# Performance work log

Hardware: AMD Instinct MI355X
Metric: run time of the kernel (lower is better)

The kernel has to match this reference:

```python
import jax, jax.numpy as jnp
import numpy as np

KV_H, Q_H, ATT_H = 256, 256, 128
B, S, SQ = 2, 1024, 512

def setup_inputs() -> dict:
    key = jax.random.key(0)
    ks = jax.random.split(key, 8)
    sc = lambda d: 1.0 / np.sqrt(d)
    return {
        "attention_kv": jax.random.normal(ks[0], (B, S, KV_H), dtype=jnp.float32),
        "attention_query": jax.random.normal(ks[1], (B, SQ, Q_H), dtype=jnp.float32),
        "W_kv": jax.random.uniform(ks[2], (KV_H, ATT_H), jnp.float32, -sc(KV_H), sc(KV_H)),
        "b_kv": jax.random.uniform(ks[3], (ATT_H,), jnp.float32, -sc(KV_H), sc(KV_H)),
        "W_q": jax.random.uniform(ks[4], (Q_H, ATT_H), jnp.float32, -sc(Q_H), sc(Q_H)),
        "b_q": jax.random.uniform(ks[5], (ATT_H,), jnp.float32, -sc(Q_H), sc(Q_H)),
        "w_v": jax.random.uniform(ks[6], (ATT_H,), jnp.float32, -sc(ATT_H), sc(ATT_H)),
        "b_v": jax.random.uniform(ks[7], (), jnp.float32, -sc(ATT_H), sc(ATT_H)),
    }

def reference(attention_kv, attention_query, W_kv, b_kv, W_q, b_q, w_v, b_v):
    # proj_kv: (B, S, A); proj_q: (B, Sq, A)
    proj_kv = jnp.einsum('bsh,ha->bsa', attention_kv, W_kv) + b_kv
    proj_q = jnp.einsum('bqh,ha->bqa', attention_query, W_q) + b_q
    # broadcast add + tanh -> (B, Sq, S, A)
    hidden = jnp.tanh(proj_kv[:, None, :, :] + proj_q[:, :, None, :])
    # scalar score per (b, q, s)
    attention_score = jnp.einsum('bqsa,a->bqs', hidden, w_v) + b_v
    attention_weight = jax.nn.softmax(attention_score, axis=-1)
    # weighted sum over kv sequence -> (B, Sq, KV_H)
    attention_output = jnp.einsum('bqs,bsh->bqh', attention_weight, attention_kv)
    return attention_output, attention_weight
```

## Files before the change

### kernel.cpp

```cpp
#include <hip/hip_runtime.h>
#include <hip/hip_bf16.h>

#define NB   2
#define SKV  1024
#define NSQ  512
#define HIN  256
#define HA   128

#define KSC   2.8853900817779268f
#define LOG2E 1.4426950408889634f

__global__ __launch_bounds__(128) void proj_kernel(
    const float* __restrict__ kv,
    const float* __restrict__ qy,
    const float* __restrict__ Wkv,
    const float* __restrict__ bkv,
    const float* __restrict__ Wq,
    const float* __restrict__ bq,
    float* __restrict__ pk,
    float* __restrict__ pq)
{
    __shared__ __align__(16) float rowf[8][HIN];
    const int t  = threadIdx.x;
    const int r0 = blockIdx.x * 8;
    const bool is_q = (r0 >= NB * SKV);
    const float* __restrict__ src = is_q ? (qy + (size_t)(r0 - NB * SKV) * HIN)
                                         : (kv + (size_t)r0 * HIN);
    const float* __restrict__ W  = is_q ? Wq : Wkv;
    const float* __restrict__ bs = is_q ? bq : bkv;
    float* __restrict__ dst = is_q ? (pq + (size_t)(r0 - NB * SKV) * HA)
                                   : (pk + (size_t)r0 * HA);

    const float4* __restrict__ s4 = (const float4*)src;
    float4* r4 = (float4*)&rowf[0][0];
    #pragma unroll
    for (int i = 0; i < 4; ++i) r4[t + i * 128] = s4[t + i * 128];
    __syncthreads();

    float a[8];
    #pragma unroll
    for (int i = 0; i < 8; ++i) a[i] = 0.f;
    #pragma unroll 4
    for (int h = 0; h < HIN; ++h) {
        float w = W[h * HA + t];
        #pragma unroll
        for (int i = 0; i < 8; ++i) a[i] = fmaf(rowf[i][h], w, a[i]);
    }
    const float bb = bs[t];
    #pragma unroll
    for (int i = 0; i < 8; ++i) dst[i * HA + t] = (a[i] + bb) * KSC;
}

__global__ __launch_bounds__(512) void attn_kernel(
    const float* __restrict__ pk,
    const float* __restrict__ pq,
    const float* __restrict__ wv,
    const float* __restrict__ bv,
    const float* __restrict__ kv,
    float* __restrict__ out)
{
    __shared__ __align__(16) float eq_s[4][HA];
    __shared__ __align__(16) float wv_s[HA];
    __shared__ __align__(16) float wt_s[SKV][4];
    __shared__ float red[2][4][8];
    __shared__ float w0red[8];
    __shared__ __align__(16) float part[8][4][HIN];

    const int tid  = threadIdx.x;
    const int lane = tid & 63, wid = tid >> 6;
    const int bq0  = blockIdx.x * 4;
    const int b    = bq0 >> 9;

    {
        const int row = tid >> 7, a = tid & 127;
        eq_s[row][a] = __builtin_amdgcn_exp2f(pq[(size_t)(bq0 + row) * HA + a]);
    }
    float w0p = (tid < HA) ? wv[tid] : 0.f;
    if (tid < HA) wv_s[tid] = w0p;
    #pragma unroll
    for (int o = 32; o > 0; o >>= 1) w0p += __shfl_down(w0p, o);
    if (lane == 0) w0red[wid] = w0p;
    const float bvf = bv[0];
    __syncthreads();
    float W0 = 0.f;
    #pragma unroll
    for (int i = 0; i < 8; ++i) W0 += w0red[i];

    float sc[4][2];
    #pragma unroll
    for (int si = 0; si < 2; ++si) {
        const int s = si * 512 + tid;
        const float4* __restrict__ prow = (const float4*)(pk + (size_t)(b * SKV + s) * HA);
        const float4* __restrict__ wv4  = (const float4*)wv_s;
        const float4* __restrict__ q40  = (const float4*)&eq_s[0][0];
        const float4* __restrict__ q41  = (const float4*)&eq_s[1][0];
        const float4* __restrict__ q42  = (const float4*)&eq_s[2][0];
        const float4* __restrict__ q43  = (const float4*)&eq_s[3][0];
        float a0 = 0.f, a1 = 0.f, a2 = 0.f, a3 = 0.f;
        #pragma unroll 4
        for (int a4 = 0; a4 < 32; ++a4) {
            const float4 p  = prow[a4];
            const float4 w4 = wv4[a4];
            float4 E;
            E.x = __builtin_amdgcn_exp2f(p.x);
            E.y = __builtin_amdgcn_exp2f(p.y);
            E.z = __builtin_amdgcn_exp2f(p.z);
            E.w = __builtin_amdgcn_exp2f(p.w);
            const float4 q0 = q40[a4];
            const float4 q1 = q41[a4];
            const float4 q2 = q42[a4];
            const float4 q3 = q43[a4];
            a0 = fmaf(w4.x, __builtin_amdgcn_rcpf(fmaf(E.x, q0.x, 1.f)), a0);
            a1 = fmaf(w4.x, __builtin_amdgcn_rcpf(fmaf(E.x, q1.x, 1.f)), a1);
            a2 = fmaf(w4.x, __builtin_amdgcn_rcpf(fmaf(E.x, q2.x, 1.f)), a2);
            a3 = fmaf(w4.x, __builtin_amdgcn_rcpf(fmaf(E.x, q3.x, 1.f)), a3);
            a0 = fmaf(w4.y, __builtin_amdgcn_rcpf(fmaf(E.y, q0.y, 1.f)), a0);
            a1 = fmaf(w4.y, __builtin_amdgcn_rcpf(fmaf(E.y, q1.y, 1.f)), a1);
            a2 = fmaf(w4.y, __builtin_amdgcn_rcpf(fmaf(E.y, q2.y, 1.f)), a2);
            a3 = fmaf(w4.y, __builtin_amdgcn_rcpf(fmaf(E.y, q3.y, 1.f)), a3);
            a0 = fmaf(w4.z, __builtin_amdgcn_rcpf(fmaf(E.z, q0.z, 1.f)), a0);
            a1 = fmaf(w4.z, __builtin_amdgcn_rcpf(fmaf(E.z, q1.z, 1.f)), a1);
            a2 = fmaf(w4.z, __builtin_amdgcn_rcpf(fmaf(E.z, q2.z, 1.f)), a2);
            a3 = fmaf(w4.z, __builtin_amdgcn_rcpf(fmaf(E.z, q3.z, 1.f)), a3);
            a0 = fmaf(w4.w, __builtin_amdgcn_rcpf(fmaf(E.w, q0.w, 1.f)), a0);
            a1 = fmaf(w4.w, __builtin_amdgcn_rcpf(fmaf(E.w, q1.w, 1.f)), a1);
            a2 = fmaf(w4.w, __builtin_amdgcn_rcpf(fmaf(E.w, q2.w, 1.f)), a2);
            a3 = fmaf(w4.w, __builtin_amdgcn_rcpf(fmaf(E.w, q3.w, 1.f)), a3);
        }
        sc[0][si] = fmaf(-2.f, a0, W0) + bvf;
        sc[1][si] = fmaf(-2.f, a1, W0) + bvf;
        sc[2][si] = fmaf(-2.f, a2, W0) + bvf;
        sc[3][si] = fmaf(-2.f, a3, W0) + bvf;
    }

    #pragma unroll
    for (int q = 0; q < 4; ++q) {
        float m = fmaxf(sc[q][0], sc[q][1]);
        #pragma unroll
        for (int o = 32; o > 0; o >>= 1) m = fmaxf(m, __shfl_down(m, o));
        if (lane == 0) red[0][q][wid] = m;
    }
    __syncthreads();
    float M[4];
    #pragma unroll
    for (int q = 0; q < 4; ++q) {
        float m = red[0][q][0];
        #pragma unroll
        for (int i = 1; i < 8; ++i) m = fmaxf(m, red[0][q][i]);
        M[q] = m;
    }
    float e[4][2];
    #pragma unroll
    for (int q = 0; q < 4; ++q) {
        e[q][0] = __builtin_amdgcn_exp2f((sc[q][0] - M[q]) * LOG2E);
        e[q][1] = __builtin_amdgcn_exp2f((sc[q][1] - M[q]) * LOG2E);
        float sum = e[q][0] + e[q][1];
        #pragma unroll
        for (int o = 32; o > 0; o >>= 1) sum += __shfl_down(sum, o);
        if (lane == 0) red[1][q][wid] = sum;
    }
    __syncthreads();
    float rw[4];
    #pragma unroll
    for (int q = 0; q < 4; ++q) {
        float d = red[1][q][0];
        #pragma unroll
        for (int i = 1; i < 8; ++i) d += red[1][q][i];
        rw[q] = 1.0f / d;
    }

    float* __restrict__ outw = out + (size_t)NB * NSQ * HIN;
    #pragma unroll
    for (int si = 0; si < 2; ++si) {
        const int s = si * 512 + tid;
        #pragma unroll
        for (int q = 0; q < 4; ++q) {
            const float w = e[q][si] * rw[q];
            wt_s[s][q] = w;
            outw[(size_t)(bq0 + q) * SKV + s] = w;
        }
    }
    __syncthreads();

    {
        const int g = wid;
        float4 ac0 = {0,0,0,0}, ac1 = {0,0,0,0}, ac2 = {0,0,0,0}, ac3 = {0,0,0,0};
        const float4* __restrict__ kvb =
            (const float4*)(kv + (size_t)(b * SKV + g * 128) * HIN);
        #pragma unroll 4
        for (int i = 0; i < 128; ++i) {
            const int s = g * 128 + i;
            const float4 w4 = *((const float4*)&wt_s[s][0]);
            const float4 v  = kvb[(size_t)i * 64 + lane];
            ac0.x = fmaf(w4.x, v.x, ac0.x); ac0.y = fmaf(w4.x, v.y, ac0.y);
            ac0.z = fmaf(w4.x, v.z, ac0.z); ac0.w = fmaf(w4.x, v.w, ac0.w);
            ac1.x = fmaf(w4.y, v.x, ac1.x); ac1.y = fmaf(w4.y, v.y, ac1.y);
            ac1.z = fmaf(w4.y, v.z, ac1.z); ac1.w = fmaf(w4.y, v.w, ac1.w);
            ac2.x = fmaf(w4.z, v.x, ac2.x); ac2.y = fmaf(w4.z, v.y, ac2.y);
            ac2.z = fmaf(w4.z, v.z, ac2.z); ac2.w = fmaf(w4.z, v.w, ac2.w);
            ac3.x = fmaf(w4.w, v.x, ac3.x); ac3.y = fmaf(w4.w, v.y, ac3.y);
            ac3.z = fmaf(w4.w, v.z, ac3.z); ac3.w = fmaf(w4.w, v.w, ac3.w);
        }
        ((float4*)part[g][0])[lane] = ac0;
        ((float4*)part[g][1])[lane] = ac1;
        ((float4*)part[g][2])[lane] = ac2;
        ((float4*)part[g][3])[lane] = ac3;
    }
    __syncthreads();
    #pragma unroll
    for (int k = 0; k < 2; ++k) {
        const int id = tid + k * 512;
        const int q = id >> 8, h = id & 255;
        float v = 0.f;
        #pragma unroll
        for (int g2 = 0; g2 < 8; ++g2) v += part[g2][q][h];
        out[(size_t)(bq0 + q) * HIN + h] = v;
    }
}

extern "C" void kernel_launch(void* const* d_in, const int* in_sizes, int n_in,
                              void* d_out, int out_size, void* d_ws, size_t ws_size,
                              hipStream_t stream) {
    (void)in_sizes; (void)n_in; (void)out_size; (void)ws_size;
    const float* kv  = (const float*)d_in[0];
    const float* qy  = (const float*)d_in[1];
    const float* Wkv = (const float*)d_in[2];
    const float* bkv = (const float*)d_in[3];
    const float* Wq  = (const float*)d_in[4];
    const float* bq  = (const float*)d_in[5];
    const float* wv  = (const float*)d_in[6];
    const float* bv  = (const float*)d_in[7];

    float* pk = (float*)d_ws;
    float* pq = pk + (size_t)NB * SKV * HA;
    float* out = (float*)d_out;

    hipLaunchKernelGGL(proj_kernel, dim3((NB * SKV + NB * NSQ) / 8), dim3(128), 0, stream,
                       kv, qy, Wkv, bkv, Wq, bq, pk, pq);
    hipLaunchKernelGGL(attn_kernel, dim3(NB * NSQ / 4), dim3(512), 0, stream,
                       pk, pq, wv, bv, kv, out);
}
```

Before: 123.4 us.

## Precompute exponentials in projection and pair reciprocals to halve rcp count

The projection kernel now applies exp2 to its outputs, so the attention kernel no longer recomputes exp of the key projections once per query block. The score loop combines two tanh terms over a common denominator, using one reciprocal per pair of elements instead of two. The attention block grows to 1024 threads with one key position per thread, and the projection reads input rows straight from global memory instead of staging them in shared memory. The paired form adds multiplies, risks overflow when the products of exponentials grow large, and the larger block may lower occupancy.

After: 118.5 us. 3.9% less time.

```diff
diff --git a/kernel.cpp b/kernel.cpp
--- a/kernel.cpp
+++ b/kernel.cpp
@@ -1,5 +1,4 @@
 #include <hip/hip_runtime.h>
-#include <hip/hip_bf16.h>
 
 #define NB   2
 #define SKV  1024
@@ -17,10 +16,9 @@
     const float* __restrict__ bkv,
     const float* __restrict__ Wq,
     const float* __restrict__ bq,
-    float* __restrict__ pk,
-    float* __restrict__ pq)
+    float* __restrict__ ek,
+    float* __restrict__ eq)
 {
-    __shared__ __align__(16) float rowf[8][HIN];
     const int t  = threadIdx.x;
     const int r0 = blockIdx.x * 8;
     const bool is_q = (r0 >= NB * SKV);
@@ -28,114 +26,98 @@
                                          : (kv + (size_t)r0 * HIN);
     const float* __restrict__ W  = is_q ? Wq : Wkv;
     const float* __restrict__ bs = is_q ? bq : bkv;
-    float* __restrict__ dst = is_q ? (pq + (size_t)(r0 - NB * SKV) * HA)
-                                   : (pk + (size_t)r0 * HA);
+    float* __restrict__ dst = is_q ? (eq + (size_t)(r0 - NB * SKV) * HA)
+                                   : (ek + (size_t)r0 * HA);
+
+    float a[8];
+    #pragma unroll
+    for (int i = 0; i < 8; ++i) a[i] = 0.f;
 
     const float4* __restrict__ s4 = (const float4*)src;
-    float4* r4 = (float4*)&rowf[0][0];
-    #pragma unroll
-    for (int i = 0; i < 4; ++i) r4[t + i * 128] = s4[t + i * 128];
-    __syncthreads();
-
-    float a[8];
-    #pragma unroll
-    for (int i = 0; i < 8; ++i) a[i] = 0.f;
-    #pragma unroll 4
-    for (int h = 0; h < HIN; ++h) {
-        float w = W[h * HA + t];
-        #pragma unroll
-        for (int i = 0; i < 8; ++i) a[i] = fmaf(rowf[i][h], w, a[i]);
+    #pragma unroll 2
+    for (int h4 = 0; h4 < 64; ++h4) {
+        float4 r[8];
+        #pragma unroll
+        for (int i = 0; i < 8; ++i) r[i] = s4[(size_t)i * 64 + h4];
+        #pragma unroll
+        for (int j = 0; j < 4; ++j) {
+            const float w = W[(size_t)(h4 * 4 + j) * HA + t];
+            #pragma unroll
+            for (int i = 0; i < 8; ++i)
+                a[i] = fmaf(((const float*)&r[i])[j], w, a[i]);
+        }
     }
     const float bb = bs[t];
     #pragma unroll
-    for (int i = 0; i < 8; ++i) dst[i * HA + t] = (a[i] + bb) * KSC;
+    for (int i = 0; i < 8; ++i)
+        dst[(size_t)i * HA + t] = __builtin_amdgcn_exp2f((a[i] + bb) * KSC);
 }
 
-__global__ __launch_bounds__(512) void attn_kernel(
-    const float* __restrict__ pk,
-    const float* __restrict__ pq,
+__global__ __launch_bounds__(1024) void attn_kernel(
+    const float* __restrict__ ek,
+    const float* __restrict__ eq,
     const float* __restrict__ wv,
     const float* __restrict__ bv,
     const float* __restrict__ kv,
     float* __restrict__ out)
 {
-    __shared__ __align__(16) float eq_s[4][HA];
-    __shared__ __align__(16) float wv_s[HA];
     __shared__ __align__(16) float wt_s[SKV][4];
-    __shared__ float red[2][4][8];
-    __shared__ float w0red[8];
-    __shared__ __align__(16) float part[8][4][HIN];
+    __shared__ __align__(16) float part[16][4][HIN];
+    __shared__ float red[2][4][16];
 
     const int tid  = threadIdx.x;
     const int lane = tid & 63, wid = tid >> 6;
     const int bq0  = blockIdx.x * 4;
     const int b    = bq0 >> 9;
 
-    {
-        const int row = tid >> 7, a = tid & 127;
-        eq_s[row][a] = __builtin_amdgcn_exp2f(pq[(size_t)(bq0 + row) * HA + a]);
-    }
-    float w0p = (tid < HA) ? wv[tid] : 0.f;
-    if (tid < HA) wv_s[tid] = w0p;
-    #pragma unroll
-    for (int o = 32; o > 0; o >>= 1) w0p += __shfl_down(w0p, o);
-    if (lane == 0) w0red[wid] = w0p;
-    const float bvf = bv[0];
-    __syncthreads();
-    float W0 = 0.f;
-    #pragma unroll
-    for (int i = 0; i < 8; ++i) W0 += w0red[i];
-
-    float sc[4][2];
-    #pragma unroll
-    for (int si = 0; si < 2; ++si) {
-        const int s = si * 512 + tid;
-        const float4* __restrict__ prow = (const float4*)(pk + (size_t)(b * SKV + s) * HA);
-        const float4* __restrict__ wv4  = (const float4*)wv_s;
-        const float4* __restrict__ q40  = (const float4*)&eq_s[0][0];
-        const float4* __restrict__ q41  = (const float4*)&eq_s[1][0];
-        const float4* __restrict__ q42  = (const float4*)&eq_s[2][0];
-        const float4* __restrict__ q43  = (const float4*)&eq_s[3][0];
-        float a0 = 0.f, a1 = 0.f, a2 = 0.f, a3 = 0.f;
-        #pragma unroll 4
-        for (int a4 = 0; a4 < 32; ++a4) {
-            const float4 p  = prow[a4];
-            const float4 w4 = wv4[a4];
-            float4 E;
-            E.x = __builtin_amdgcn_exp2f(p.x);
-            E.y = __builtin_amdgcn_exp2f(p.y);
-            E.z = __builtin_amdgcn_exp2f(p.z);
-            E.w = __builtin_amdgcn_exp2f(p.w);
-            const float4 q0 = q40[a4];
-            const float4 q1 = q41[a4];
-            const float4 q2 = q42[a4];
-            const float4 q3 = q43[a4];
-            a0 = fmaf(w4.x, __builtin_amdgcn_rcpf(fmaf(E.x, q0.x, 1.f)), a0);
-            a1 = fmaf(w4.x, __builtin_amdgcn_rcpf(fmaf(E.x, q1.x, 1.f)), a1);
-            a2 = fmaf(w4.x, __builtin_amdgcn_rcpf(fmaf(E.x, q2.x, 1.f)), a2);
-            a3 = fmaf(w4.x, __builtin_amdgcn_rcpf(fmaf(E.x, q3.x, 1.f)), a3);
-            a0 = fmaf(w4.y, __builtin_amdgcn_rcpf(fmaf(E.y, q0.y, 1.f)), a0);
-            a1 = fmaf(w4.y, __builtin_amdgcn_rcpf(fmaf(E.y, q1.y, 1.f)), a1);
-            a2 = fmaf(w4.y, __builtin_amdgcn_rcpf(fmaf(E.y, q2.y, 1.f)), a2);
-            a3 = fmaf(w4.y, __builtin_amdgcn_rcpf(fmaf(E.y, q3.y, 1.f)), a3);
-            a0 = fmaf(w4.z, __builtin_amdgcn_rcpf(fmaf(E.z, q0.z, 1.f)), a0);
-            a1 = fmaf(w4.z, __builtin_amdgcn_rcpf(fmaf(E.z, q1.z, 1.f)), a1);
-            a2 = fmaf(w4.z, __builtin_amdgcn_rcpf(fmaf(E.z, q2.z, 1.f)), a2);
-            a3 = fmaf(w4.z, __builtin_amdgcn_rcpf(fmaf(E.z, q3.z, 1.f)), a3);
-            a0 = fmaf(w4.w, __builtin_amdgcn_rcpf(fmaf(E.w, q0.w, 1.f)), a0);
-            a1 = fmaf(w4.w, __builtin_amdgcn_rcpf(fmaf(E.w, q1.w, 1.f)), a1);
-            a2 = fmaf(w4.w, __builtin_amdgcn_rcpf(fmaf(E.w, q2.w, 1.f)), a2);
-            a3 = fmaf(w4.w, __builtin_amdgcn_rcpf(fmaf(E.w, q3.w, 1.f)), a3);
+    const float4* __restrict__ eq4 = (const float4*)(eq + (size_t)bq0 * HA);
+    const float4* __restrict__ wv4 = (const float4*)wv;
+
+    float W0 = bv[0];
+    #pragma unroll 8
+    for (int i = 0; i < 32; ++i) {
+        const float4 w = wv4[i];
+        W0 += (w.x + w.y) + (w.z + w.w);
+    }
+
+    const int s = tid;
+    const float4* __restrict__ ek4 =
+        (const float4*)(ek + ((size_t)(b * SKV + s)) * HA);
+    float acc0 = 0.f, acc1 = 0.f, acc2 = 0.f, acc3 = 0.f;
+
+    #pragma unroll 4
+    for (int a4 = 0; a4 < 32; ++a4) {
+        const float4 E = ek4[a4];
+        const float4 w = wv4[a4];
+
+#define PAIR_Q(ACC, QIDX)                                                     \
+        {                                                                     \
+            const float4 Q = eq4[(QIDX) * 32 + a4];      \
+            float u  = fmaf(E.x, Q.x, 1.f);                                   \
+            float v  = fmaf(E.y, Q.y, 1.f);                                   \
+            float n  = fmaf(w.x, v, w.y * u);                                 \
+            ACC = fmaf(n, __builtin_amdgcn_rcpf(u * v), ACC);                 \
+            float u2 = fmaf(E.z, Q.z, 1.f);                                   \
+            float v2 = fmaf(E.w, Q.w, 1.f);                                   \
+            float n2 = fmaf(w.z, v2, w.w * u2);                               \
+            ACC = fmaf(n2, __builtin_amdgcn_rcpf(u2 * v2), ACC);              \
         }
-        sc[0][si] = fmaf(-2.f, a0, W0) + bvf;
-        sc[1][si] = fmaf(-2.f, a1, W0) + bvf;
-        sc[2][si] = fmaf(-2.f, a2, W0) + bvf;
-        sc[3][si] = fmaf(-2.f, a3, W0) + bvf;
-    }
-
-    #pragma unroll
-    for (int q = 0; q < 4; ++q) {
-        float m = fmaxf(sc[q][0], sc[q][1]);
+        PAIR_Q(acc0, 0)
+        PAIR_Q(acc1, 1)
+        PAIR_Q(acc2, 2)
+        PAIR_Q(acc3, 3)
+#undef PAIR_Q
+    }
+
+    float sc[4];
+    sc[0] = fmaf(-2.f, acc0, W0);
+    sc[1] = fmaf(-2.f, acc1, W0);
+    sc[2] = fmaf(-2.f, acc2, W0);
+    sc[3] = fmaf(-2.f, acc3, W0);
+
+    #pragma unroll
+    for (int q = 0; q < 4; ++q) {
+        float m = sc[q];
         #pragma unroll
         for (int o = 32; o > 0; o >>= 1) m = fmaxf(m, __shfl_down(m, o));
         if (lane == 0) red[0][q][wid] = m;
@@ -146,51 +128,43 @@
     for (int q = 0; q < 4; ++q) {
         float m = red[0][q][0];
         #pragma unroll
-        for (int i = 1; i < 8; ++i) m = fmaxf(m, red[0][q][i]);
+        for (int i = 1; i < 16; ++i) m = fmaxf(m, red[0][q][i]);
         M[q] = m;
     }
-    float e[4][2];
-    #pragma unroll
-    for (int q = 0; q < 4; ++q) {
-        e[q][0] = __builtin_amdgcn_exp2f((sc[q][0] - M[q]) * LOG2E);
-        e[q][1] = __builtin_amdgcn_exp2f((sc[q][1] - M[q]) * LOG2E);
-        float sum = e[q][0] + e[q][1];
+    float e[4];
+    #pragma unroll
+    for (int q = 0; q < 4; ++q) {
+        e[q] = __builtin_amdgcn_exp2f((sc[q] - M[q]) * LOG2E);
+        float sum = e[q];
         #pragma unroll
         for (int o = 32; o > 0; o >>= 1) sum += __shfl_down(sum, o);
         if (lane == 0) red[1][q][wid] = sum;
     }
     __syncthreads();
-    float rw[4];
+    float wgt[4];
     #pragma unroll
     for (int q = 0; q < 4; ++q) {
         float d = red[1][q][0];
         #pragma unroll
-        for (int i = 1; i < 8; ++i) d += red[1][q][i];
-        rw[q] = 1.0f / d;
+        for (int i = 1; i < 16; ++i) d += red[1][q][i];
+        wgt[q] = e[q] * __builtin_amdgcn_rcpf(d);
     }
 
     float* __restrict__ outw = out + (size_t)NB * NSQ * HIN;
-    #pragma unroll
-    for (int si = 0; si < 2; ++si) {
-        const int s = si * 512 + tid;
-        #pragma unroll
-        for (int q = 0; q < 4; ++q) {
-            const float w = e[q][si] * rw[q];
-            wt_s[s][q] = w;
-            outw[(size_t)(bq0 + q) * SKV + s] = w;
-        }
-    }
+    *(float4*)&wt_s[s][0] = make_float4(wgt[0], wgt[1], wgt[2], wgt[3]);
+    #pragma unroll
+    for (int q = 0; q < 4; ++q)
+        outw[(size_t)(bq0 + q) * SKV + s] = wgt[q];
     __syncthreads();
 
     {
         const int g = wid;
         float4 ac0 = {0,0,0,0}, ac1 = {0,0,0,0}, ac2 = {0,0,0,0}, ac3 = {0,0,0,0};
         const float4* __restrict__ kvb =
-            (const float4*)(kv + (size_t)(b * SKV + g * 128) * HIN);
+            (const float4*)(kv + (size_t)(b * SKV + g * 64) * HIN);
         #pragma unroll 4
-        for (int i = 0; i < 128; ++i) {
-            const int s = g * 128 + i;
-            const float4 w4 = *((const float4*)&wt_s[s][0]);
+        for (int i = 0; i < 64; ++i) {
+            const float4 w4 = *((const float4*)&wt_s[g * 64 + i][0]);
             const float4 v  = kvb[(size_t)i * 64 + lane];
             ac0.x = fmaf(w4.x, v.x, ac0.x); ac0.y = fmaf(w4.x, v.y, ac0.y);
             ac0.z = fmaf(w4.x, v.z, ac0.z); ac0.w = fmaf(w4.x, v.w, ac0.w);
@@ -207,13 +181,11 @@
         ((float4*)part[g][3])[lane] = ac3;
     }
     __syncthreads();
-    #pragma unroll
-    for (int k = 0; k < 2; ++k) {
-        const int id = tid + k * 512;
-        const int q = id >> 8, h = id & 255;
+    {
+        const int q = tid >> 8, h = tid & 255;
         float v = 0.f;
         #pragma unroll
-        for (int g2 = 0; g2 < 8; ++g2) v += part[g2][q][h];
+        for (int g2 = 0; g2 < 16; ++g2) v += part[g2][q][h];
         out[(size_t)(bq0 + q) * HIN + h] = v;
     }
 }
@@ -231,12 +203,12 @@
     const float* wv  = (const float*)d_in[6];
     const float* bv  = (const float*)d_in[7];
 
-    float* pk = (float*)d_ws;
-    float* pq = pk + (size_t)NB * SKV * HA;
+    float* ek = (float*)d_ws;
+    float* eqp = ek + (size_t)NB * SKV * HA;
     float* out = (float*)d_out;
 
     hipLaunchKernelGGL(proj_kernel, dim3((NB * SKV + NB * NSQ) / 8), dim3(128), 0, stream,
-                       kv, qy, Wkv, bkv, Wq, bq, pk, pq);
-    hipLaunchKernelGGL(attn_kernel, dim3(NB * NSQ / 4), dim3(512), 0, stream,
-                       pk, pq, wv, bv, kv, out);
+                       kv, qy, Wkv, bkv, Wq, bq, ek, eqp);
+    hipLaunchKernelGGL(attn_kernel, dim3(NB * NSQ / 4), dim3(1024), 0, stream,
+                       ek, eqp, wv, bv, kv, out);
 }
```
